# Kernel optimization log

Measured on AMD Instinct MI355X. Metric: run time of the kernel, lower is better.

Reference implementation:

```python
import jax, jax.numpy as jnp
import numpy as np

B, T = 32, 512
IN, D, H, HD, L, FFN = 375, 512, 8, 64, 6, 1024
NC, CD, LAT, K = 4, 64, 256, 512
DL, DH, DFF, OUT = 4, 512, 1024, 291


def setup_inputs() -> dict:
    key = jax.random.key(0)
    ks = iter(jax.random.split(key, 64))
    def p(shape, scale=0.02):
        return jax.random.normal(next(ks), shape, jnp.float32) * scale
    return {
        "x": jax.random.normal(next(ks), (B, T, IN), jnp.float32),
        "in_w": p((IN, D)), "in_b": jnp.zeros((D,), jnp.float32),
        "enc_ln1_s": jnp.ones((L, D), jnp.float32), "enc_ln1_b": jnp.zeros((L, D), jnp.float32),
        "enc_qkv_w": p((L, D, 3 * D)), "enc_qkv_b": jnp.zeros((L, 3 * D), jnp.float32),
        "enc_out_w": p((L, D, D)), "enc_out_b": jnp.zeros((L, D), jnp.float32),
        "enc_ln2_s": jnp.ones((L, D), jnp.float32), "enc_ln2_b": jnp.zeros((L, D), jnp.float32),
        "enc_ff1_w": p((L, D, FFN)), "enc_ff1_b": jnp.zeros((L, FFN), jnp.float32),
        "enc_ff2_w": p((L, FFN, D)), "enc_ff2_b": jnp.zeros((L, D), jnp.float32),
        "lat_w": p((D, LAT)), "lat_b": jnp.zeros((LAT,), jnp.float32),
        "codebook": jax.random.uniform(next(ks), (K, CD), jnp.float32, -1.0 / K, 1.0 / K),
        "unlat_w": p((LAT, DH)), "unlat_b": jnp.zeros((DH,), jnp.float32),
        "dec_ln_s": jnp.ones((DL, DH), jnp.float32), "dec_ln_b": jnp.zeros((DL, DH), jnp.float32),
        "dec_ff1_w": p((DL, DH, DFF)), "dec_ff1_b": jnp.zeros((DL, DFF), jnp.float32),
        "dec_ff2_w": p((DL, DFF, DH)), "dec_ff2_b": jnp.zeros((DL, DH), jnp.float32),
        "out_w": p((DH, OUT)), "out_b": jnp.zeros((OUT,), jnp.float32),
    }


def _ln(x, s, b):
    m = x.mean(-1, keepdims=True)
    v = jnp.var(x, axis=-1, keepdims=True)
    return (x - m) / jnp.sqrt(v + 1e-5) * s + b


def _rope(x, cos, sin):
    # interleaved even/odd rotation, matches torch stack(...,-1).flatten(-2)
    xe, xo = x[..., 0::2], x[..., 1::2]
    re = xe * cos - xo * sin
    ro = xe * sin + xo * cos
    return jnp.stack((re, ro), axis=-1).reshape(x.shape)


def _forward(x, in_w, in_b, enc_ln1_s, enc_ln1_b, enc_qkv_w, enc_qkv_b,
             enc_out_w, enc_out_b, enc_ln2_s, enc_ln2_b, enc_ff1_w, enc_ff1_b,
             enc_ff2_w, enc_ff2_b, lat_w, lat_b, codebook, unlat_w, unlat_b,
             dec_ln_s, dec_ln_b, dec_ff1_w, dec_ff1_b, dec_ff2_w, dec_ff2_b,
             out_w, out_b):
    h = x @ in_w + in_b  # [B,T,D]
    inv_freq = 1.0 / (10000.0 ** (jnp.arange(0, HD, 2, dtype=jnp.float32) / HD))
    freqs = jnp.outer(jnp.arange(T, dtype=jnp.float32), inv_freq)  # [T, HD/2]
    cos, sin = jnp.cos(freqs), jnp.sin(freqs)
    for i in range(L):
        y = _ln(h, enc_ln1_s[i], enc_ln1_b[i])
        qkv = (y @ enc_qkv_w[i] + enc_qkv_b[i]).reshape(B, T, 3, H, HD)
        qkv = qkv.transpose(2, 0, 3, 1, 4)  # [3,B,H,T,HD]
        q, k, v = qkv[0], qkv[1], qkv[2]
        q = _rope(q, cos, sin)
        k = _rope(k, cos, sin)
        sc = jnp.einsum('bhqd,bhkd->bhqk', q, k) / np.float32(np.sqrt(HD))
        probs = jax.nn.softmax(sc, axis=-1)
        a = jnp.einsum('bhqk,bhkd->bhqd', probs, v)
        a = a.transpose(0, 2, 1, 3).reshape(B, T, D)
        h = h + (a @ enc_out_w[i] + enc_out_b[i])
        y = _ln(h, enc_ln2_s[i], enc_ln2_b[i])
        h = h + (jax.nn.gelu(y @ enc_ff1_w[i] + enc_ff1_b[i], approximate=False)
                 @ enc_ff2_w[i] + enc_ff2_b[i])
    # VQ bottleneck: split each token latent into NC subvectors, nearest code each
    z_bt = (h @ lat_w + lat_b).reshape(B * T, LAT)
    flat_z = z_bt.reshape(-1, CD)  # [B*T*NC, CD]
    d = ((flat_z ** 2).sum(1, keepdims=True)
         - 2.0 * (flat_z @ codebook.T)
         + (codebook ** 2).sum(1))  # [B*T*NC, K]
    idx = jnp.argmin(d, axis=1)
    q_bt = codebook[idx].reshape(B * T, LAT)
    st = z_bt + jax.lax.stop_gradient(q_bt - z_bt)  # straight-through
    g = st.reshape(B, T, LAT) @ unlat_w + unlat_b
    for i in range(DL):
        y = _ln(g, dec_ln_s[i], dec_ln_b[i])
        g = g + (jax.nn.gelu(y @ dec_ff1_w[i] + dec_ff1_b[i], approximate=False)
                 @ dec_ff2_w[i] + dec_ff2_b[i])
    return g @ out_w + out_b  # [B,T,291]


def reference(x, in_w, in_b, enc_ln1_s, enc_ln1_b, enc_qkv_w, enc_qkv_b,
              enc_out_w, enc_out_b, enc_ln2_s, enc_ln2_b, enc_ff1_w, enc_ff1_b,
              enc_ff2_w, enc_ff2_b, lat_w, lat_b, codebook, unlat_w, unlat_b,
              dec_ln_s, dec_ln_b, dec_ff1_w, dec_ff1_b, dec_ff2_w, dec_ff2_b,
              out_w, out_b):
    return _forward(x, in_w, in_b, enc_ln1_s, enc_ln1_b, enc_qkv_w, enc_qkv_b,
                    enc_out_w, enc_out_b, enc_ln2_s, enc_ln2_b, enc_ff1_w, enc_ff1_b,
                    enc_ff2_w, enc_ff2_b, lat_w, lat_b, codebook, unlat_w, unlat_b,
                    dec_ln_s, dec_ln_b, dec_ff1_w, dec_ff1_b, dec_ff2_w, dec_ff2_b,
                    out_w, out_b)
```

## Files before the change

kernel.cpp:

```cpp
#include <hip/hip_runtime.h>
#include <hip/hip_bf16.h>

#define BB 32
#define TT 512
#define IND 375
#define DD 512
#define HH 8
#define HDD 64
#define LL 6
#define FFNN 1024
#define LATD 256
#define KCODES 512
#define DLL 4
#define DHH 512
#define DFFF 1024
#define OUTD 291
#define MTOK (BB*TT)
#define KPAD 384
#define NPAD 384

__global__ void rope_table_k(float* __restrict__ cosb, float* __restrict__ sinb) {
  int idx = blockIdx.x * blockDim.x + threadIdx.x;
  if (idx >= TT * 32) return;
  int t = idx >> 5, i = idx & 31;
  float inv = powf(10000.0f, -(float)(2 * i) / 64.0f);
  float f = (float)t * inv;
  cosb[idx] = cosf(f);
  sinb[idx] = sinf(f);
}

__global__ void pad_x_k(const float* __restrict__ x, float* __restrict__ Xp) {
  int m = blockIdx.x;
  const float* src = x + (size_t)m * IND;
  float* dst = Xp + (size_t)m * KPAD;
  for (int k = threadIdx.x; k < KPAD; k += 256)
    dst[k] = (k < IND) ? src[k] : 0.0f;
}
__global__ void pad_wx_k(const float* __restrict__ w, float* __restrict__ Wp) {
  int e = blockIdx.x * 256 + threadIdx.x;
  if (e >= KPAD * DD) return;
  int k = e >> 9, n = e & 511;
  Wp[e] = (k < IND) ? w[(size_t)k * DD + n] : 0.0f;
}
__global__ void pad_wo_k(const float* __restrict__ w, const float* __restrict__ b,
                         float* __restrict__ Wp, float* __restrict__ bp) {
  int e = blockIdx.x * 256 + threadIdx.x;
  if (e >= DHH * NPAD) return;
  int k = e / NPAD, n = e - k * NPAD;
  Wp[e] = (n < OUTD) ? w[(size_t)k * OUTD + n] : 0.0f;
  if (e < NPAD) bp[e] = (e < OUTD) ? b[e] : 0.0f;
}
__global__ void unpad_k(const float* __restrict__ Cp, float* __restrict__ out) {
  int m = blockIdx.x;
  const float* src = Cp + (size_t)m * NPAD;
  float* dst = out + (size_t)m * OUTD;
  for (int n = threadIdx.x; n < OUTD; n += 256)
    dst[n] = src[n];
}

template<int EPI>
__global__ __launch_bounds__(256) void gemm128_k(const float* __restrict__ A,
                                                 const float* __restrict__ W,
                                                 const float* __restrict__ bias,
                                                 const float* __restrict__ R,
                                                 float* __restrict__ C,
                                                 int M, int K, int N,
                                                 const float* __restrict__ COS,
                                                 const float* __restrict__ SIN) {
  __shared__ float As[32][128];
  __shared__ float4 Bs4[32][2][16];
  const int bn = blockIdx.x * 128;
  const int bm = blockIdx.y * 128;
  const int tid = threadIdx.x;
  const int tx = tid & 15;
  const int ty = tid >> 4;
  const int ar = tid >> 1;
  const int ak = (tid & 1) * 16;
  const int bk = tid >> 3;
  const int bxs = tid & 7;

  float acc[8][8] = {};

  for (int k0 = 0; k0 < K; k0 += 32) {
    const float* ap = A + (size_t)(bm + ar) * K + k0 + ak;
    float4 a0 = *(const float4*)ap;
    float4 a1 = *(const float4*)(ap + 4);
    float4 a2 = *(const float4*)(ap + 8);
    float4 a3 = *(const float4*)(ap + 12);
    const float* bp = W + (size_t)(k0 + bk) * N + bn + bxs * 16;
    float4 b0 = *(const float4*)bp;
    float4 b1 = *(const float4*)(bp + 4);
    float4 b2 = *(const float4*)(bp + 8);
    float4 b3 = *(const float4*)(bp + 12);

    __syncthreads();
    As[ak +  0][ar] = a0.x; As[ak +  1][ar] = a0.y; As[ak +  2][ar] = a0.z; As[ak +  3][ar] = a0.w;
    As[ak +  4][ar] = a1.x; As[ak +  5][ar] = a1.y; As[ak +  6][ar] = a1.z; As[ak +  7][ar] = a1.w;
    As[ak +  8][ar] = a2.x; As[ak +  9][ar] = a2.y; As[ak + 10][ar] = a2.z; As[ak + 11][ar] = a2.w;
    As[ak + 12][ar] = a3.x; As[ak + 13][ar] = a3.y; As[ak + 14][ar] = a3.z; As[ak + 15][ar] = a3.w;
    Bs4[bk][0][2 * bxs]     = b0;
    Bs4[bk][1][2 * bxs]     = b1;
    Bs4[bk][0][2 * bxs + 1] = b2;
    Bs4[bk][1][2 * bxs + 1] = b3;
    __syncthreads();

#pragma unroll
    for (int kk = 0; kk < 32; ++kk) {
      float4 va0 = *(const float4*)&As[kk][ty * 8];
      float4 va1 = *(const float4*)&As[kk][ty * 8 + 4];
      float4 vb0 = Bs4[kk][0][tx];
      float4 vb1 = Bs4[kk][1][tx];
      float av[8] = {va0.x, va0.y, va0.z, va0.w, va1.x, va1.y, va1.z, va1.w};
      float bv[8] = {vb0.x, vb0.y, vb0.z, vb0.w, vb1.x, vb1.y, vb1.z, vb1.w};
#pragma unroll
      for (int ii = 0; ii < 8; ++ii)
#pragma unroll
        for (int jj = 0; jj < 8; ++jj)
          acc[ii][jj] = __builtin_fmaf(av[ii], bv[jj], acc[ii][jj]);
    }
  }

#pragma unroll
  for (int ii = 0; ii < 8; ++ii) {
    int m = bm + ty * 8 + ii;
#pragma unroll
    for (int g = 0; g < 2; ++g) {
      int n0 = bn + tx * 8 + g * 4;
      float t4[4];
#pragma unroll
      for (int j = 0; j < 4; ++j) {
        float v = acc[ii][g * 4 + j] + bias[n0 + j];
        if (EPI == 1) v += R[(size_t)m * N + n0 + j];
        if (EPI == 2) v = 0.5f * v * (1.0f + erff(v * 0.70710678118654752f));
        t4[j] = v;
      }
      if (EPI == 3 && n0 < 2 * DD) {
        int tpos = m & 511;
        int i0 = (n0 & 63) >> 1;
        float c0 = COS[tpos * 32 + i0],     s0 = SIN[tpos * 32 + i0];
        float c1 = COS[tpos * 32 + i0 + 1], s1 = SIN[tpos * 32 + i0 + 1];
        float xe0 = t4[0], xo0 = t4[1], xe1 = t4[2], xo1 = t4[3];
        t4[0] = xe0 * c0 - xo0 * s0;
        t4[1] = xe0 * s0 + xo0 * c0;
        t4[2] = xe1 * c1 - xo1 * s1;
        t4[3] = xe1 * s1 + xo1 * c1;
      }
      float4 vv; vv.x = t4[0]; vv.y = t4[1]; vv.z = t4[2]; vv.w = t4[3];
      *(float4*)&C[(size_t)m * N + n0] = vv;
    }
  }
}

__global__ __launch_bounds__(256) void ln_k(const float* __restrict__ X,
                                            const float* __restrict__ s,
                                            const float* __restrict__ b,
                                            float* __restrict__ Y) {
  int wave = threadIdx.x >> 6, lane = threadIdx.x & 63;
  int row = blockIdx.x * 4 + wave;
  const float* x = X + (size_t)row * DD;
  float v[8];
  float sum = 0.0f;
#pragma unroll
  for (int j = 0; j < 8; ++j) { v[j] = x[lane + 64 * j]; sum += v[j]; }
#pragma unroll
  for (int o = 32; o; o >>= 1) sum += __shfl_xor(sum, o);
  float mean = sum * (1.0f / 512.0f);
  float var = 0.0f;
#pragma unroll
  for (int j = 0; j < 8; ++j) { float d = v[j] - mean; var += d * d; }
#pragma unroll
  for (int o = 32; o; o >>= 1) var += __shfl_xor(var, o);
  float inv = 1.0f / sqrtf(var * (1.0f / 512.0f) + 1e-5f);
  float* y = Y + (size_t)row * DD;
#pragma unroll
  for (int j = 0; j < 8; ++j) {
    int d = lane + 64 * j;
    y[d] = (v[j] - mean) * inv * s[d] + b[d];
  }
}

__global__ __launch_bounds__(256) void fattn_k(const float* __restrict__ qkv,
                                               float* __restrict__ out) {
  __shared__ float Qs[64][68];
  __shared__ float KVs[64][68];
  __shared__ float Ps[64][68];
  const int tid = threadIdx.x;
  const int tx = tid & 15, ty = tid >> 4;
  const int g = blockIdx.x;
  const int xcd = g & 7, slot = g >> 3;
  const int qt = slot & 7;
  const int p = ((slot >> 3) << 3) | xcd;
  const int h = p & 7;
  const int b = p >> 3;
  const float* base = qkv + (size_t)b * TT * (3 * DD) + h * HDD;

  {
    int r = tid & 63, q0 = tid >> 6;
#pragma unroll
    for (int jj = 0; jj < 4; ++jj) {
      int q = q0 + jj * 4;
      float4 v = *(const float4*)(base + (size_t)(qt * 64 + r) * (3 * DD) + q * 4);
      Qs[q * 4 + 0][r] = v.x; Qs[q * 4 + 1][r] = v.y;
      Qs[q * 4 + 2][r] = v.z; Qs[q * 4 + 3][r] = v.w;
    }
  }

  float o[4][4] = {};
  float m[4] = {-1e30f, -1e30f, -1e30f, -1e30f};
  float l[4] = {0.f, 0.f, 0.f, 0.f};

  for (int kt = 0; kt < 8; ++kt) {
    __syncthreads();
    {
      int r = tid & 63, q0 = tid >> 6;
#pragma unroll
      for (int jj = 0; jj < 4; ++jj) {
        int q = q0 + jj * 4;
        float4 v = *(const float4*)(base + (size_t)(kt * 64 + r) * (3 * DD) + DD + q * 4);
        KVs[q * 4 + 0][r] = v.x; KVs[q * 4 + 1][r] = v.y;
        KVs[q * 4 + 2][r] = v.z; KVs[q * 4 + 3][r] = v.w;
      }
    }
    __syncthreads();

    float s[4][4] = {};
#pragma unroll 4
    for (int d = 0; d < 64; ++d) {
      float4 a4 = *(const float4*)&Qs[d][ty * 4];
      float4 b4 = *(const float4*)&KVs[d][tx * 4];
      float av[4] = {a4.x, a4.y, a4.z, a4.w};
      float bv[4] = {b4.x, b4.y, b4.z, b4.w};
#pragma unroll
      for (int ii = 0; ii < 4; ++ii)
#pragma unroll
        for (int jj = 0; jj < 4; ++jj)
          s[ii][jj] = __builtin_fmaf(av[ii], bv[jj], s[ii][jj]);
    }

#pragma unroll
    for (int i = 0; i < 4; ++i) {
      float mm = fmaxf(fmaxf(s[i][0], s[i][1]), fmaxf(s[i][2], s[i][3])) * 0.125f;
#pragma unroll
      for (int off = 1; off < 16; off <<= 1) mm = fmaxf(mm, __shfl_xor(mm, off));
      float mn = fmaxf(m[i], mm);
      float f = expf(m[i] - mn);
      m[i] = mn;
      float ls = 0.0f;
#pragma unroll
      for (int j = 0; j < 4; ++j) {
        float pp = expf(__builtin_fmaf(s[i][j], 0.125f, -mn));
        s[i][j] = pp;
        ls += pp;
      }
#pragma unroll
      for (int off = 1; off < 16; off <<= 1) ls += __shfl_xor(ls, off);
      l[i] = __builtin_fmaf(l[i], f, ls);
#pragma unroll
      for (int j = 0; j < 4; ++j) o[i][j] *= f;
    }

    __syncthreads();

#pragma unroll
    for (int j = 0; j < 4; ++j) {
      float4 pv; pv.x = s[0][j]; pv.y = s[1][j]; pv.z = s[2][j]; pv.w = s[3][j];
      *(float4*)&Ps[tx * 4 + j][ty * 4] = pv;
    }
#pragma unroll
    for (int ii = 0; ii < 4; ++ii) {
      int e = tid + 256 * ii;
      int c = e >> 4, q = e & 15;
      float4 v = *(const float4*)(base + (size_t)(kt * 64 + c) * (3 * DD) + 2 * DD + q * 4);
      *(float4*)&KVs[c][q * 4] = v;
    }
    __syncthreads();

#pragma unroll 4
    for (int c = 0; c < 64; ++c) {
      float4 a4 = *(const float4*)&Ps[c][ty * 4];
      float4 b4 = *(const float4*)&KVs[c][tx * 4];
      float av[4] = {a4.x, a4.y, a4.z, a4.w};
      float bv[4] = {b4.x, b4.y, b4.z, b4.w};
#pragma unroll
      for (int ii = 0; ii < 4; ++ii)
#pragma unroll
        for (int jj = 0; jj < 4; ++jj)
          o[ii][jj] = __builtin_fmaf(av[ii], bv[jj], o[ii][jj]);
    }
  }

#pragma unroll
  for (int i = 0; i < 4; ++i) {
    float inv = 1.0f / l[i];
    int tok = b * TT + qt * 64 + ty * 4 + i;
    float4 vv;
    vv.x = o[i][0] * inv; vv.y = o[i][1] * inv;
    vv.z = o[i][2] * inv; vv.w = o[i][3] * inv;
    *(float4*)&out[(size_t)tok * DD + h * HDD + tx * 4] = vv;
  }
}

__device__ __forceinline__ float npsumsq64(const float* __restrict__ a) {
  float r0 = __fmul_rn(a[0], a[0]), r1 = __fmul_rn(a[1], a[1]);
  float r2 = __fmul_rn(a[2], a[2]), r3 = __fmul_rn(a[3], a[3]);
  float r4 = __fmul_rn(a[4], a[4]), r5 = __fmul_rn(a[5], a[5]);
  float r6 = __fmul_rn(a[6], a[6]), r7 = __fmul_rn(a[7], a[7]);
#pragma unroll
  for (int i = 8; i < 64; i += 8) {
    r0 = __fadd_rn(r0, __fmul_rn(a[i + 0], a[i + 0]));
    r1 = __fadd_rn(r1, __fmul_rn(a[i + 1], a[i + 1]));
    r2 = __fadd_rn(r2, __fmul_rn(a[i + 2], a[i + 2]));
    r3 = __fadd_rn(r3, __fmul_rn(a[i + 3], a[i + 3]));
    r4 = __fadd_rn(r4, __fmul_rn(a[i + 4], a[i + 4]));
    r5 = __fadd_rn(r5, __fmul_rn(a[i + 5], a[i + 5]));
    r6 = __fadd_rn(r6, __fmul_rn(a[i + 6], a[i + 6]));
    r7 = __fadd_rn(r7, __fmul_rn(a[i + 7], a[i + 7]));
  }
  return __fadd_rn(__fadd_rn(__fadd_rn(r0, r1), __fadd_rn(r2, r3)),
                   __fadd_rn(__fadd_rn(r4, r5), __fadd_rn(r6, r7)));
}

__global__ void vqs2_k(const float* __restrict__ CB, float* __restrict__ S2) {
  int k = blockIdx.x * 256 + threadIdx.x;
  if (k < KCODES) S2[k] = npsumsq64(CB + (size_t)k * 64);
}

__global__ __launch_bounds__(256) void vq32b_k(const float* __restrict__ Z,
                                               const float* __restrict__ CB,
                                               const float* __restrict__ S2,
                                               int* __restrict__ idxOut) {
  __shared__ float zs[16][68];
  __shared__ float cs[64][68];
  __shared__ float s2s[64];
  __shared__ float rv[256];
  __shared__ int   ri[256];
  const int tid = threadIdx.x;
  const int lr = tid >> 4;
  const int sub = tid & 15;
  const int row0 = blockIdx.x * 16;

  {
    int r = tid >> 4, q = tid & 15;
    *(float4*)&zs[r][q * 4] = *(const float4*)(Z + (size_t)(row0 + r) * 64 + q * 4);
  }
  __syncthreads();

  const float S1 = npsumsq64(zs[lr]);

  float bv = 3.4e38f;
  int bi = 0x7fffffff;
  for (int ct = 0; ct < 8; ++ct) {
    __syncthreads();
    for (int e = tid; e < 1024; e += 256) {
      int r = e >> 4, q = e & 15;
      *(float4*)&cs[r][q * 4] = *(const float4*)(CB + (size_t)(ct * 64 + r) * 64 + q * 4);
    }
    if (tid < 64) s2s[tid] = S2[ct * 64 + tid];
    __syncthreads();
#pragma unroll
    for (int cc = 0; cc < 4; ++cc) {
      int kl = cc * 16 + sub;
      float g = 0.0f;
#pragma unroll
      for (int d4 = 0; d4 < 16; ++d4) {
        float4 zf = *(const float4*)&zs[lr][d4 * 4];
        float4 cf = *(const float4*)&cs[kl][d4 * 4];
        g = __builtin_fmaf(zf.x, cf.x, g);
        g = __builtin_fmaf(zf.y, cf.y, g);
        g = __builtin_fmaf(zf.z, cf.z, g);
        g = __builtin_fmaf(zf.w, cf.w, g);
      }
      float d32 = __fadd_rn(__fsub_rn(S1, __fmul_rn(2.0f, g)), s2s[kl]);
      int k = ct * 64 + kl;
      if (d32 < bv || (d32 == bv && k < bi)) { bv = d32; bi = k; }
    }
  }
  rv[tid] = bv; ri[tid] = bi;
  __syncthreads();
  if (sub == 0) {
    float bb = rv[tid]; int ii = ri[tid];
#pragma unroll
    for (int j = 1; j < 16; ++j) {
      float v = rv[tid + j]; int id = ri[tid + j];
      if (v < bb || (v == bb && id < ii)) { bb = v; ii = id; }
    }
    idxOut[row0 + lr] = ii;
  }
}

__global__ void stgather_k(const float* __restrict__ Z, const float* __restrict__ CB,
                           const int* __restrict__ idx, float* __restrict__ Q) {
  int e = blockIdx.x * blockDim.x + threadIdx.x;
  if (e >= MTOK * LATD) return;
  int chunk = e >> 6, d = e & 63;
  int k = idx[chunk] & (KCODES - 1);
  float z = Z[e];
  float c = CB[(size_t)k * 64 + d];
  Q[e] = __fadd_rn(z, __fsub_rn(c, z));
}

static inline dim3 g128(int M, int N) { return dim3(N / 128, M / 128); }

extern "C" void kernel_launch(void* const* d_in, const int* in_sizes, int n_in,
                              void* d_out, int out_size, void* d_ws, size_t ws_size,
                              hipStream_t stream) {
  const float* x        = (const float*)d_in[0];
  const float* in_w     = (const float*)d_in[1];
  const float* in_b     = (const float*)d_in[2];
  const float* ln1_s    = (const float*)d_in[3];
  const float* ln1_b    = (const float*)d_in[4];
  const float* qkv_w    = (const float*)d_in[5];
  const float* qkv_b    = (const float*)d_in[6];
  const float* aout_w   = (const float*)d_in[7];
  const float* aout_b   = (const float*)d_in[8];
  const float* ln2_s    = (const float*)d_in[9];
  const float* ln2_b    = (const float*)d_in[10];
  const float* ff1_w    = (const float*)d_in[11];
  const float* ff1_b    = (const float*)d_in[12];
  const float* ff2_w    = (const float*)d_in[13];
  const float* ff2_b    = (const float*)d_in[14];
  const float* lat_w    = (const float*)d_in[15];
  const float* lat_b    = (const float*)d_in[16];
  const float* codebook = (const float*)d_in[17];
  const float* unlat_w  = (const float*)d_in[18];
  const float* unlat_b  = (const float*)d_in[19];
  const float* dln_s    = (const float*)d_in[20];
  const float* dln_b    = (const float*)d_in[21];
  const float* dff1_w   = (const float*)d_in[22];
  const float* dff1_b   = (const float*)d_in[23];
  const float* dff2_w   = (const float*)d_in[24];
  const float* dff2_b   = (const float*)d_in[25];
  const float* ow       = (const float*)d_in[26];
  const float* ob       = (const float*)d_in[27];
  float* out = (float*)d_out;

  float* ws   = (float*)d_ws;
  float* Hb   = ws;
  float* Yb   = Hb + (size_t)MTOK * DD;
  float* QKVb = Yb + (size_t)MTOK * DD;
  float* COSb = QKVb + (size_t)MTOK * 3 * DD;
  float* SINb = COSb + TT * 32;
  int*   IDXb = (int*)(SINb + TT * 32);
  float* S2b  = (float*)(IDXb + MTOK * 4);
  float* WXp  = S2b + KCODES;
  float* WOp  = WXp + (size_t)KPAD * DD;
  float* BOp  = WOp + (size_t)DHH * NPAD;
  float* Xp   = QKVb;
  float* Cp   = QKVb;

  dim3 blk(256);

  rope_table_k<<<(TT * 32 + 255) / 256, blk, 0, stream>>>(COSb, SINb);
  vqs2_k<<<2, blk, 0, stream>>>(codebook, S2b);
  pad_wx_k<<<(KPAD * DD + 255) / 256, blk, 0, stream>>>(in_w, WXp);
  pad_wo_k<<<(DHH * NPAD + 255) / 256, blk, 0, stream>>>(ow, ob, WOp, BOp);
  pad_x_k<<<MTOK, blk, 0, stream>>>(x, Xp);

  gemm128_k<0><<<g128(MTOK, DD), blk, 0, stream>>>(Xp, WXp, in_b, nullptr, Hb,
                                                   MTOK, KPAD, DD, nullptr, nullptr);

  for (int l = 0; l < LL; ++l) {
    ln_k<<<MTOK / 4, blk, 0, stream>>>(Hb, ln1_s + l * DD, ln1_b + l * DD, Yb);
    gemm128_k<3><<<g128(MTOK, 3 * DD), blk, 0, stream>>>(Yb, qkv_w + (size_t)l * DD * 3 * DD,
                                                         qkv_b + l * 3 * DD, nullptr, QKVb,
                                                         MTOK, DD, 3 * DD, COSb, SINb);
    fattn_k<<<BB * HH * (TT / 64), blk, 0, stream>>>(QKVb, Yb);
    gemm128_k<1><<<g128(MTOK, DD), blk, 0, stream>>>(Yb, aout_w + (size_t)l * DD * DD,
                                                     aout_b + l * DD, Hb, Hb, MTOK, DD, DD,
                                                     nullptr, nullptr);
    ln_k<<<MTOK / 4, blk, 0, stream>>>(Hb, ln2_s + l * DD, ln2_b + l * DD, Yb);
    gemm128_k<2><<<g128(MTOK, FFNN), blk, 0, stream>>>(Yb, ff1_w + (size_t)l * DD * FFNN,
                                                       ff1_b + l * FFNN, nullptr, QKVb,
                                                       MTOK, DD, FFNN, nullptr, nullptr);
    gemm128_k<1><<<g128(MTOK, DD), blk, 0, stream>>>(QKVb, ff2_w + (size_t)l * FFNN * DD,
                                                     ff2_b + l * DD, Hb, Hb, MTOK, FFNN, DD,
                                                     nullptr, nullptr);
  }

  gemm128_k<0><<<g128(MTOK, LATD), blk, 0, stream>>>(Hb, lat_w, lat_b, nullptr, Yb,
                                                     MTOK, DD, LATD, nullptr, nullptr);
  vq32b_k<<<(MTOK * 4) / 16, blk, 0, stream>>>(Yb, codebook, S2b, IDXb);
  stgather_k<<<(MTOK * LATD) / 256, blk, 0, stream>>>(Yb, codebook, IDXb, QKVb);
  gemm128_k<0><<<g128(MTOK, DHH), blk, 0, stream>>>(QKVb, unlat_w, unlat_b, nullptr, Hb,
                                                    MTOK, LATD, DHH, nullptr, nullptr);

  for (int l = 0; l < DLL; ++l) {
    ln_k<<<MTOK / 4, blk, 0, stream>>>(Hb, dln_s + l * DHH, dln_b + l * DHH, Yb);
    gemm128_k<2><<<g128(MTOK, DFFF), blk, 0, stream>>>(Yb, dff1_w + (size_t)l * DHH * DFFF,
                                                       dff1_b + l * DFFF, nullptr, QKVb,
                                                       MTOK, DHH, DFFF, nullptr, nullptr);
    gemm128_k<1><<<g128(MTOK, DHH), blk, 0, stream>>>(QKVb, dff2_w + (size_t)l * DFFF * DHH,
                                                      dff2_b + l * DHH, Hb, Hb, MTOK, DFFF, DHH,
                                                      nullptr, nullptr);
  }

  gemm128_k<0><<<g128(MTOK, NPAD), blk, 0, stream>>>(Hb, WOp, BOp, nullptr, Cp,
                                                     MTOK, DHH, NPAD, nullptr, nullptr);
  unpad_k<<<MTOK, blk, 0, stream>>>(Cp, out);
}
```

Before: 8.868 ms.

## Use split-bf16 MFMA GEMM for decoder and output projections

Adds a bf16x3 (hi/lo split) MFMA GEMM kernel and routes the unlatent, decoder FFN and output projections through it, with weights pre-split and transposed into bf16 hi/lo buffers. A tiles are split on the fly while being staged into LDS. The aim is to replace the scalar fp32 FMA GEMM with matrix-core throughput while keeping near-fp32 accuracy. The cost is extra split kernels per call, three MFMAs per product, and more workspace; the encoder GEMMs stay on the old path.

```diff
diff --git a/kernel.cpp b/kernel.cpp
--- a/kernel.cpp
+++ b/kernel.cpp
@@ -19,6 +19,18 @@
 #define KPAD 384
 #define NPAD 384
 
+typedef short short8v __attribute__((ext_vector_type(8)));
+typedef float float4v __attribute__((ext_vector_type(4)));
+
+__device__ __forceinline__ unsigned short f2bf(float f) {
+  unsigned int u = __float_as_uint(f);
+  unsigned int r = (u + 0x7FFFu + ((u >> 16) & 1u)) >> 16;
+  return (unsigned short)r;
+}
+__device__ __forceinline__ float bf2f(unsigned short s) {
+  return __uint_as_float(((unsigned int)s) << 16);
+}
+
 __global__ void rope_table_k(float* __restrict__ cosb, float* __restrict__ sinb) {
   int idx = blockIdx.x * blockDim.x + threadIdx.x;
   if (idx >= TT * 32) return;
@@ -56,6 +68,18 @@
   float* dst = out + (size_t)m * OUTD;
   for (int n = threadIdx.x; n < OUTD; n += 256)
     dst[n] = src[n];
+}
+
+__global__ void wsplit_k(const float* __restrict__ w, unsigned short* __restrict__ hiT,
+                         unsigned short* __restrict__ loT, int K, int N) {
+  int e = blockIdx.x * 256 + threadIdx.x;
+  if (e >= K * N) return;
+  int k = e / N, n = e - k * N;
+  float a = w[e];
+  unsigned short h = f2bf(a);
+  unsigned short l = f2bf(a - bf2f(h));
+  hiT[(size_t)n * K + k] = h;
+  loT[(size_t)n * K + k] = l;
 }
 
 template<int EPI>
@@ -147,6 +171,101 @@
       }
       float4 vv; vv.x = t4[0]; vv.y = t4[1]; vv.z = t4[2]; vv.w = t4[3];
       *(float4*)&C[(size_t)m * N + n0] = vv;
+    }
+  }
+}
+
+template<int EPI>
+__global__ __launch_bounds__(256) void bgemm_k(const float* __restrict__ A,
+                                               const unsigned short* __restrict__ BhiT,
+                                               const unsigned short* __restrict__ BloT,
+                                               const float* __restrict__ bias,
+                                               const float* __restrict__ R,
+                                               float* __restrict__ C,
+                                               int M, int K, int N) {
+  __shared__ unsigned short Ah[128][40];
+  __shared__ unsigned short Al[128][40];
+  __shared__ unsigned short Bh[128][40];
+  __shared__ unsigned short Bl[128][40];
+  const int bn = blockIdx.x * 128;
+  const int bm = blockIdx.y * 128;
+  const int tid = threadIdx.x;
+  const int w = tid >> 6, lane = tid & 63;
+  const int wm = (w >> 1) * 64, wn = (w & 1) * 64;
+  const int lr = lane & 15;
+  const int kh = lane >> 4;
+
+  const int sr = tid >> 1;
+  const int sk = (tid & 1) * 16;
+
+  float4v acc[4][4] = {};
+
+  for (int k0 = 0; k0 < K; k0 += 32) {
+    const float* ap = A + (size_t)(bm + sr) * K + k0 + sk;
+    float av[16];
+#pragma unroll
+    for (int q = 0; q < 4; ++q) {
+      float4 v = *(const float4*)(ap + q * 4);
+      av[q * 4 + 0] = v.x; av[q * 4 + 1] = v.y; av[q * 4 + 2] = v.z; av[q * 4 + 3] = v.w;
+    }
+    const unsigned short* bph = BhiT + (size_t)(bn + sr) * K + k0 + sk;
+    const unsigned short* bpl = BloT + (size_t)(bn + sr) * K + k0 + sk;
+    uint4 bh0 = *(const uint4*)bph, bh1 = *(const uint4*)(bph + 8);
+    uint4 bl0 = *(const uint4*)bpl, bl1 = *(const uint4*)(bpl + 8);
+
+    __syncthreads();
+    unsigned int hw[8], lw[8];
+#pragma unroll
+    for (int q = 0; q < 8; ++q) {
+      unsigned short h0 = f2bf(av[2 * q]);
+      unsigned short l0 = f2bf(av[2 * q] - bf2f(h0));
+      unsigned short h1 = f2bf(av[2 * q + 1]);
+      unsigned short l1 = f2bf(av[2 * q + 1] - bf2f(h1));
+      hw[q] = (unsigned int)h0 | ((unsigned int)h1 << 16);
+      lw[q] = (unsigned int)l0 | ((unsigned int)l1 << 16);
+    }
+    *(uint4*)&Ah[sr][sk]     = make_uint4(hw[0], hw[1], hw[2], hw[3]);
+    *(uint4*)&Ah[sr][sk + 8] = make_uint4(hw[4], hw[5], hw[6], hw[7]);
+    *(uint4*)&Al[sr][sk]     = make_uint4(lw[0], lw[1], lw[2], lw[3]);
+    *(uint4*)&Al[sr][sk + 8] = make_uint4(lw[4], lw[5], lw[6], lw[7]);
+    *(uint4*)&Bh[sr][sk]     = bh0;
+    *(uint4*)&Bh[sr][sk + 8] = bh1;
+    *(uint4*)&Bl[sr][sk]     = bl0;
+    *(uint4*)&Bl[sr][sk + 8] = bl1;
+    __syncthreads();
+
+    short8v bfh[4], bfl[4];
+#pragma unroll
+    for (int nt = 0; nt < 4; ++nt) {
+      bfh[nt] = *(const short8v*)&Bh[wn + nt * 16 + lr][kh * 8];
+      bfl[nt] = *(const short8v*)&Bl[wn + nt * 16 + lr][kh * 8];
+    }
+#pragma unroll
+    for (int mt = 0; mt < 4; ++mt) {
+      short8v afh = *(const short8v*)&Ah[wm + mt * 16 + lr][kh * 8];
+      short8v afl = *(const short8v*)&Al[wm + mt * 16 + lr][kh * 8];
+#pragma unroll
+      for (int nt = 0; nt < 4; ++nt) {
+        acc[mt][nt] = __builtin_amdgcn_mfma_f32_16x16x32_bf16(afh, bfh[nt], acc[mt][nt], 0, 0, 0);
+        acc[mt][nt] = __builtin_amdgcn_mfma_f32_16x16x32_bf16(afh, bfl[nt], acc[mt][nt], 0, 0, 0);
+        acc[mt][nt] = __builtin_amdgcn_mfma_f32_16x16x32_bf16(afl, bfh[nt], acc[mt][nt], 0, 0, 0);
+      }
+    }
+  }
+
+#pragma unroll
+  for (int mt = 0; mt < 4; ++mt) {
+#pragma unroll
+    for (int nt = 0; nt < 4; ++nt) {
+#pragma unroll
+      for (int r = 0; r < 4; ++r) {
+        int row = bm + wm + mt * 16 + (lane >> 4) * 4 + r;
+        int col = bn + wn + nt * 16 + (lane & 15);
+        float v = acc[mt][nt][r] + bias[col];
+        if (EPI == 1) v += R[(size_t)row * N + col];
+        if (EPI == 2) v = 0.5f * v * (1.0f + erff(v * 0.70710678118654752f));
+        C[(size_t)row * N + col] = v;
+      }
     }
   }
 }
@@ -445,8 +564,17 @@
   float* WXp  = S2b + KCODES;
   float* WOp  = WXp + (size_t)KPAD * DD;
   float* BOp  = WOp + (size_t)DHH * NPAD;
-  float* Xp   = QKVb;
-  float* Cp   = QKVb;
+  unsigned short* u0  = (unsigned short*)(BOp + NPAD);
+  unsigned short* UH  = u0;
+  unsigned short* UL  = UH + (size_t)DHH * LATD;
+  unsigned short* F1H = UL + (size_t)DHH * LATD;
+  unsigned short* F1L = F1H + (size_t)DLL * DFFF * DHH;
+  unsigned short* F2H = F1L + (size_t)DLL * DFFF * DHH;
+  unsigned short* F2L = F2H + (size_t)DLL * DHH * DFFF;
+  unsigned short* OH  = F2L + (size_t)DLL * DHH * DFFF;
+  unsigned short* OL  = OH + (size_t)NPAD * DHH;
+  float* Xp = QKVb;
+  float* Cp = QKVb;
 
   dim3 blk(256);
 
@@ -455,6 +583,17 @@
   pad_wx_k<<<(KPAD * DD + 255) / 256, blk, 0, stream>>>(in_w, WXp);
   pad_wo_k<<<(DHH * NPAD + 255) / 256, blk, 0, stream>>>(ow, ob, WOp, BOp);
   pad_x_k<<<MTOK, blk, 0, stream>>>(x, Xp);
+
+  wsplit_k<<<(LATD * DHH + 255) / 256, blk, 0, stream>>>(unlat_w, UH, UL, LATD, DHH);
+  for (int l = 0; l < DLL; ++l) {
+    wsplit_k<<<(DHH * DFFF + 255) / 256, blk, 0, stream>>>(
+        dff1_w + (size_t)l * DHH * DFFF, F1H + (size_t)l * DFFF * DHH,
+        F1L + (size_t)l * DFFF * DHH, DHH, DFFF);
+    wsplit_k<<<(DFFF * DHH + 255) / 256, blk, 0, stream>>>(
+        dff2_w + (size_t)l * DFFF * DHH, F2H + (size_t)l * DHH * DFFF,
+        F2L + (size_t)l * DHH * DFFF, DFFF, DHH);
+  }
+  wsplit_k<<<(DHH * NPAD + 255) / 256, blk, 0, stream>>>(WOp, OH, OL, DHH, NPAD);
 
   gemm128_k<0><<<g128(MTOK, DD), blk, 0, stream>>>(Xp, WXp, in_b, nullptr, Hb,
                                                    MTOK, KPAD, DD, nullptr, nullptr);
@@ -481,20 +620,21 @@
                                                      MTOK, DD, LATD, nullptr, nullptr);
   vq32b_k<<<(MTOK * 4) / 16, blk, 0, stream>>>(Yb, codebook, S2b, IDXb);
   stgather_k<<<(MTOK * LATD) / 256, blk, 0, stream>>>(Yb, codebook, IDXb, QKVb);
-  gemm128_k<0><<<g128(MTOK, DHH), blk, 0, stream>>>(QKVb, unlat_w, unlat_b, nullptr, Hb,
-                                                    MTOK, LATD, DHH, nullptr, nullptr);
-
+
+  bgemm_k<0><<<g128(MTOK, DHH), blk, 0, stream>>>(QKVb, UH, UL, unlat_b, nullptr, Hb,
+                                                  MTOK, LATD, DHH);
   for (int l = 0; l < DLL; ++l) {
     ln_k<<<MTOK / 4, blk, 0, stream>>>(Hb, dln_s + l * DHH, dln_b + l * DHH, Yb);
-    gemm128_k<2><<<g128(MTOK, DFFF), blk, 0, stream>>>(Yb, dff1_w + (size_t)l * DHH * DFFF,
-                                                       dff1_b + l * DFFF, nullptr, QKVb,
-                                                       MTOK, DHH, DFFF, nullptr, nullptr);
-    gemm128_k<1><<<g128(MTOK, DHH), blk, 0, stream>>>(QKVb, dff2_w + (size_t)l * DFFF * DHH,
-                                                      dff2_b + l * DHH, Hb, Hb, MTOK, DFFF, DHH,
-                                                      nullptr, nullptr);
-  }
-
-  gemm128_k<0><<<g128(MTOK, NPAD), blk, 0, stream>>>(Hb, WOp, BOp, nullptr, Cp,
-                                                     MTOK, DHH, NPAD, nullptr, nullptr);
+    bgemm_k<2><<<g128(MTOK, DFFF), blk, 0, stream>>>(Yb, F1H + (size_t)l * DFFF * DHH,
+                                                     F1L + (size_t)l * DFFF * DHH,
+                                                     dff1_b + l * DFFF, nullptr, QKVb,
+                                                     MTOK, DHH, DFFF);
+    bgemm_k<1><<<g128(MTOK, DHH), blk, 0, stream>>>(QKVb, F2H + (size_t)l * DHH * DFFF,
+                                                    F2L + (size_t)l * DHH * DFFF,
+                                                    dff2_b + l * DHH, Hb, Hb,
+                                                    MTOK, DFFF, DHH);
+  }
+  bgemm_k<0><<<g128(MTOK, NPAD), blk, 0, stream>>>(Hb, OH, OL, BOp, nullptr, Cp,
+                                                   MTOK, DHH, NPAD);
   unpad_k<<<MTOK, blk, 0, stream>>>(Cp, out);
 }
```

After: 7.821 ms (median of 2 runs). 1.13x faster.

## Emulate fp32 GEMMs with three-way bf16 split on MFMA

Applied to the files above, without the earlier changes.

Adds a bf16x3 split-precision GEMM that decomposes activations on the fly and weights in a pre-pass into three bf16 planes, then accumulates six MFMA cross products in fp32. All dense layers use this path when the workspace is large enough, with the old fp32 SIMT GEMM kept as a fallback. The aim is to move GEMM work off vector ALUs onto matrix cores. The cost is extra weight conversion kernels each call, a large workspace, and a small accuracy difference from dropping the lowest-order terms.

```diff
diff --git a/kernel.cpp b/kernel.cpp
--- a/kernel.cpp
+++ b/kernel.cpp
@@ -19,6 +19,18 @@
 #define KPAD 384
 #define NPAD 384
 
+typedef short short8v __attribute__((ext_vector_type(8)));
+typedef float float4v __attribute__((ext_vector_type(4)));
+
+__device__ __forceinline__ unsigned short f2bf(float f) {
+  unsigned int u = __float_as_uint(f);
+  unsigned int r = (u + 0x7FFFu + ((u >> 16) & 1u)) >> 16;
+  return (unsigned short)r;
+}
+__device__ __forceinline__ float bf2f(unsigned short s) {
+  return __uint_as_float(((unsigned int)s) << 16);
+}
+
 __global__ void rope_table_k(float* __restrict__ cosb, float* __restrict__ sinb) {
   int idx = blockIdx.x * blockDim.x + threadIdx.x;
   if (idx >= TT * 32) return;
@@ -56,6 +68,23 @@
   float* dst = out + (size_t)m * OUTD;
   for (int n = threadIdx.x; n < OUTD; n += 256)
     dst[n] = src[n];
+}
+
+__global__ void wsplit3_k(const float* __restrict__ w, unsigned short* __restrict__ o,
+                          size_t planeSz, int K, int N) {
+  int e = blockIdx.x * 256 + threadIdx.x;
+  if (e >= K * N) return;
+  int k = e / N, n = e - k * N;
+  float a = w[e];
+  unsigned short h0 = f2bf(a);
+  float r = a - bf2f(h0);
+  unsigned short h1 = f2bf(r);
+  float r2 = r - bf2f(h1);
+  unsigned short h2 = f2bf(r2);
+  size_t off = (size_t)n * K + k;
+  o[off] = h0;
+  o[planeSz + off] = h1;
+  o[2 * planeSz + off] = h2;
 }
 
 template<int EPI>
@@ -147,6 +176,121 @@
       }
       float4 vv; vv.x = t4[0]; vv.y = t4[1]; vv.z = t4[2]; vv.w = t4[3];
       *(float4*)&C[(size_t)m * N + n0] = vv;
+    }
+  }
+}
+
+template<int EPI>
+__global__ __launch_bounds__(256) void bgemm6_k(const float* __restrict__ A,
+                                                const unsigned short* __restrict__ BT,
+                                                size_t planeSz,
+                                                const float* __restrict__ bias,
+                                                const float* __restrict__ R,
+                                                float* __restrict__ C,
+                                                int M, int K, int N,
+                                                const float* __restrict__ COS,
+                                                const float* __restrict__ SIN) {
+  __shared__ unsigned short A0s[128][40], A1s[128][40], A2s[128][40];
+  __shared__ unsigned short B0s[128][40], B1s[128][40], B2s[128][40];
+  const int bn = blockIdx.x * 128;
+  const int bm = blockIdx.y * 128;
+  const int tid = threadIdx.x;
+  const int w = tid >> 6, lane = tid & 63;
+  const int wm = (w >> 1) * 64, wn = (w & 1) * 64;
+  const int lr = lane & 15;
+  const int kh = lane >> 4;
+  const int sr = tid >> 1;
+  const int sk = (tid & 1) * 16;
+
+  float4v acc[4][4] = {};
+
+  for (int k0 = 0; k0 < K; k0 += 32) {
+    const float* ap = A + (size_t)(bm + sr) * K + k0 + sk;
+    float av[16];
+#pragma unroll
+    for (int q = 0; q < 4; ++q) {
+      float4 v = *(const float4*)(ap + q * 4);
+      av[q * 4 + 0] = v.x; av[q * 4 + 1] = v.y; av[q * 4 + 2] = v.z; av[q * 4 + 3] = v.w;
+    }
+    const unsigned short* b0p = BT + (size_t)(bn + sr) * K + k0 + sk;
+    uint4 b00 = *(const uint4*)b0p, b01 = *(const uint4*)(b0p + 8);
+    const unsigned short* b1p = b0p + planeSz;
+    uint4 b10 = *(const uint4*)b1p, b11 = *(const uint4*)(b1p + 8);
+    const unsigned short* b2p = b1p + planeSz;
+    uint4 b20 = *(const uint4*)b2p, b21 = *(const uint4*)(b2p + 8);
+
+    __syncthreads();
+    unsigned int w0[8], w1[8], w2[8];
+#pragma unroll
+    for (int q = 0; q < 8; ++q) {
+      float aa = av[2 * q], ab = av[2 * q + 1];
+      unsigned short h0a = f2bf(aa); float ra = aa - bf2f(h0a);
+      unsigned short h1a = f2bf(ra); float r2a = ra - bf2f(h1a);
+      unsigned short h2a = f2bf(r2a);
+      unsigned short h0b = f2bf(ab); float rb = ab - bf2f(h0b);
+      unsigned short h1b = f2bf(rb); float r2b = rb - bf2f(h1b);
+      unsigned short h2b = f2bf(r2b);
+      w0[q] = (unsigned int)h0a | ((unsigned int)h0b << 16);
+      w1[q] = (unsigned int)h1a | ((unsigned int)h1b << 16);
+      w2[q] = (unsigned int)h2a | ((unsigned int)h2b << 16);
+    }
+    *(uint4*)&A0s[sr][sk]     = make_uint4(w0[0], w0[1], w0[2], w0[3]);
+    *(uint4*)&A0s[sr][sk + 8] = make_uint4(w0[4], w0[5], w0[6], w0[7]);
+    *(uint4*)&A1s[sr][sk]     = make_uint4(w1[0], w1[1], w1[2], w1[3]);
+    *(uint4*)&A1s[sr][sk + 8] = make_uint4(w1[4], w1[5], w1[6], w1[7]);
+    *(uint4*)&A2s[sr][sk]     = make_uint4(w2[0], w2[1], w2[2], w2[3]);
+    *(uint4*)&A2s[sr][sk + 8] = make_uint4(w2[4], w2[5], w2[6], w2[7]);
+    *(uint4*)&B0s[sr][sk]     = b00;  *(uint4*)&B0s[sr][sk + 8] = b01;
+    *(uint4*)&B1s[sr][sk]     = b10;  *(uint4*)&B1s[sr][sk + 8] = b11;
+    *(uint4*)&B2s[sr][sk]     = b20;  *(uint4*)&B2s[sr][sk + 8] = b21;
+    __syncthreads();
+
+    short8v b0f[4], b1f[4], b2f[4];
+#pragma unroll
+    for (int nt = 0; nt < 4; ++nt) {
+      b0f[nt] = *(const short8v*)&B0s[wn + nt * 16 + lr][kh * 8];
+      b1f[nt] = *(const short8v*)&B1s[wn + nt * 16 + lr][kh * 8];
+      b2f[nt] = *(const short8v*)&B2s[wn + nt * 16 + lr][kh * 8];
+    }
+#pragma unroll
+    for (int mt = 0; mt < 4; ++mt) {
+      short8v a0f = *(const short8v*)&A0s[wm + mt * 16 + lr][kh * 8];
+      short8v a1f = *(const short8v*)&A1s[wm + mt * 16 + lr][kh * 8];
+      short8v a2f = *(const short8v*)&A2s[wm + mt * 16 + lr][kh * 8];
+#pragma unroll
+      for (int nt = 0; nt < 4; ++nt) {
+        acc[mt][nt] = __builtin_amdgcn_mfma_f32_16x16x32_bf16(a0f, b0f[nt], acc[mt][nt], 0, 0, 0);
+        acc[mt][nt] = __builtin_amdgcn_mfma_f32_16x16x32_bf16(a0f, b1f[nt], acc[mt][nt], 0, 0, 0);
+        acc[mt][nt] = __builtin_amdgcn_mfma_f32_16x16x32_bf16(a1f, b0f[nt], acc[mt][nt], 0, 0, 0);
+        acc[mt][nt] = __builtin_amdgcn_mfma_f32_16x16x32_bf16(a0f, b2f[nt], acc[mt][nt], 0, 0, 0);
+        acc[mt][nt] = __builtin_amdgcn_mfma_f32_16x16x32_bf16(a1f, b1f[nt], acc[mt][nt], 0, 0, 0);
+        acc[mt][nt] = __builtin_amdgcn_mfma_f32_16x16x32_bf16(a2f, b0f[nt], acc[mt][nt], 0, 0, 0);
+      }
+    }
+  }
+
+#pragma unroll
+  for (int mt = 0; mt < 4; ++mt) {
+#pragma unroll
+    for (int nt = 0; nt < 4; ++nt) {
+      int col = bn + wn + nt * 16 + (lane & 15);
+#pragma unroll
+      for (int r = 0; r < 4; ++r) {
+        int row = bm + wm + mt * 16 + (lane >> 4) * 4 + r;
+        float v = acc[mt][nt][r] + bias[col];
+        if (EPI == 1) v += R[(size_t)row * N + col];
+        if (EPI == 2) v = 0.5f * v * (1.0f + erff(v * 0.70710678118654752f));
+        if (EPI == 3) {
+          float p = __shfl_xor(v, 1);
+          if (col < 2 * DD) {
+            int tpos = row & 511;
+            int i0 = (col & 63) >> 1;
+            float c = COS[tpos * 32 + i0], s = SIN[tpos * 32 + i0];
+            v = ((col & 1) == 0) ? (v * c - p * s) : (p * s + v * c);
+          }
+        }
+        C[(size_t)row * N + col] = v;
+      }
     }
   }
 }
@@ -448,6 +592,29 @@
   float* Xp   = QKVb;
   float* Cp   = QKVb;
 
+  uintptr_t ua = ((uintptr_t)(BOp + NPAD) + 15) & ~(uintptr_t)15;
+  unsigned short* Uw = (unsigned short*)ua;
+  const size_t QWp = (size_t)(3 * DD) * DD;
+  const size_t AWp = (size_t)DD * DD;
+  const size_t F1p = (size_t)DFFF * DHH;
+  const size_t F2p = (size_t)DHH * DFFF;
+  const size_t INp = (size_t)DD * KPAD;
+  const size_t LTp = (size_t)LATD * DD;
+  const size_t UWp = (size_t)DHH * LATD;
+  const size_t OWp = (size_t)NPAD * DHH;
+  unsigned short* QW  = Uw;
+  unsigned short* AW  = QW  + 6 * 3 * QWp;
+  unsigned short* F1  = AW  + 6 * 3 * AWp;
+  unsigned short* F2  = F1  + 6 * 3 * F1p;
+  unsigned short* INW = F2  + 6 * 3 * F2p;
+  unsigned short* LTW = INW + 3 * INp;
+  unsigned short* UW  = LTW + 3 * LTp;
+  unsigned short* D1  = UW  + 3 * UWp;
+  unsigned short* D2  = D1  + 4 * 3 * F1p;
+  unsigned short* OW  = D2  + 4 * 3 * F2p;
+  size_t need = (size_t)((char*)(OW + 3 * OWp) - (char*)d_ws) + 64;
+  const bool mf = ws_size >= need;
+
   dim3 blk(256);
 
   rope_table_k<<<(TT * 32 + 255) / 256, blk, 0, stream>>>(COSb, SINb);
@@ -456,45 +623,103 @@
   pad_wo_k<<<(DHH * NPAD + 255) / 256, blk, 0, stream>>>(ow, ob, WOp, BOp);
   pad_x_k<<<MTOK, blk, 0, stream>>>(x, Xp);
 
-  gemm128_k<0><<<g128(MTOK, DD), blk, 0, stream>>>(Xp, WXp, in_b, nullptr, Hb,
-                                                   MTOK, KPAD, DD, nullptr, nullptr);
-
-  for (int l = 0; l < LL; ++l) {
-    ln_k<<<MTOK / 4, blk, 0, stream>>>(Hb, ln1_s + l * DD, ln1_b + l * DD, Yb);
-    gemm128_k<3><<<g128(MTOK, 3 * DD), blk, 0, stream>>>(Yb, qkv_w + (size_t)l * DD * 3 * DD,
-                                                         qkv_b + l * 3 * DD, nullptr, QKVb,
-                                                         MTOK, DD, 3 * DD, COSb, SINb);
-    fattn_k<<<BB * HH * (TT / 64), blk, 0, stream>>>(QKVb, Yb);
-    gemm128_k<1><<<g128(MTOK, DD), blk, 0, stream>>>(Yb, aout_w + (size_t)l * DD * DD,
-                                                     aout_b + l * DD, Hb, Hb, MTOK, DD, DD,
-                                                     nullptr, nullptr);
-    ln_k<<<MTOK / 4, blk, 0, stream>>>(Hb, ln2_s + l * DD, ln2_b + l * DD, Yb);
-    gemm128_k<2><<<g128(MTOK, FFNN), blk, 0, stream>>>(Yb, ff1_w + (size_t)l * DD * FFNN,
-                                                       ff1_b + l * FFNN, nullptr, QKVb,
-                                                       MTOK, DD, FFNN, nullptr, nullptr);
-    gemm128_k<1><<<g128(MTOK, DD), blk, 0, stream>>>(QKVb, ff2_w + (size_t)l * FFNN * DD,
-                                                     ff2_b + l * DD, Hb, Hb, MTOK, FFNN, DD,
-                                                     nullptr, nullptr);
-  }
-
-  gemm128_k<0><<<g128(MTOK, LATD), blk, 0, stream>>>(Hb, lat_w, lat_b, nullptr, Yb,
-                                                     MTOK, DD, LATD, nullptr, nullptr);
-  vq32b_k<<<(MTOK * 4) / 16, blk, 0, stream>>>(Yb, codebook, S2b, IDXb);
-  stgather_k<<<(MTOK * LATD) / 256, blk, 0, stream>>>(Yb, codebook, IDXb, QKVb);
-  gemm128_k<0><<<g128(MTOK, DHH), blk, 0, stream>>>(QKVb, unlat_w, unlat_b, nullptr, Hb,
-                                                    MTOK, LATD, DHH, nullptr, nullptr);
-
-  for (int l = 0; l < DLL; ++l) {
-    ln_k<<<MTOK / 4, blk, 0, stream>>>(Hb, dln_s + l * DHH, dln_b + l * DHH, Yb);
-    gemm128_k<2><<<g128(MTOK, DFFF), blk, 0, stream>>>(Yb, dff1_w + (size_t)l * DHH * DFFF,
-                                                       dff1_b + l * DFFF, nullptr, QKVb,
-                                                       MTOK, DHH, DFFF, nullptr, nullptr);
-    gemm128_k<1><<<g128(MTOK, DHH), blk, 0, stream>>>(QKVb, dff2_w + (size_t)l * DFFF * DHH,
-                                                      dff2_b + l * DHH, Hb, Hb, MTOK, DFFF, DHH,
+  if (mf) {
+    for (int l = 0; l < LL; ++l) {
+      wsplit3_k<<<(int)((DD * 3 * DD + 255) / 256), blk, 0, stream>>>(
+          qkv_w + (size_t)l * DD * 3 * DD, QW + (size_t)l * 3 * QWp, QWp, DD, 3 * DD);
+      wsplit3_k<<<(int)((DD * DD + 255) / 256), blk, 0, stream>>>(
+          aout_w + (size_t)l * DD * DD, AW + (size_t)l * 3 * AWp, AWp, DD, DD);
+      wsplit3_k<<<(int)((DD * FFNN + 255) / 256), blk, 0, stream>>>(
+          ff1_w + (size_t)l * DD * FFNN, F1 + (size_t)l * 3 * F1p, F1p, DD, FFNN);
+      wsplit3_k<<<(int)((FFNN * DD + 255) / 256), blk, 0, stream>>>(
+          ff2_w + (size_t)l * FFNN * DD, F2 + (size_t)l * 3 * F2p, F2p, FFNN, DD);
+    }
+    wsplit3_k<<<(int)((KPAD * DD + 255) / 256), blk, 0, stream>>>(WXp, INW, INp, KPAD, DD);
+    wsplit3_k<<<(int)((DD * LATD + 255) / 256), blk, 0, stream>>>(lat_w, LTW, LTp, DD, LATD);
+    wsplit3_k<<<(int)((LATD * DHH + 255) / 256), blk, 0, stream>>>(unlat_w, UW, UWp, LATD, DHH);
+    for (int l = 0; l < DLL; ++l) {
+      wsplit3_k<<<(int)((DHH * DFFF + 255) / 256), blk, 0, stream>>>(
+          dff1_w + (size_t)l * DHH * DFFF, D1 + (size_t)l * 3 * F1p, F1p, DHH, DFFF);
+      wsplit3_k<<<(int)((DFFF * DHH + 255) / 256), blk, 0, stream>>>(
+          dff2_w + (size_t)l * DFFF * DHH, D2 + (size_t)l * 3 * F2p, F2p, DFFF, DHH);
+    }
+    wsplit3_k<<<(int)((DHH * NPAD + 255) / 256), blk, 0, stream>>>(WOp, OW, OWp, DHH, NPAD);
+
+    bgemm6_k<0><<<g128(MTOK, DD), blk, 0, stream>>>(Xp, INW, INp, in_b, nullptr, Hb,
+                                                    MTOK, KPAD, DD, nullptr, nullptr);
+    for (int l = 0; l < LL; ++l) {
+      ln_k<<<MTOK / 4, blk, 0, stream>>>(Hb, ln1_s + l * DD, ln1_b + l * DD, Yb);
+      bgemm6_k<3><<<g128(MTOK, 3 * DD), blk, 0, stream>>>(Yb, QW + (size_t)l * 3 * QWp, QWp,
+                                                          qkv_b + l * 3 * DD, nullptr, QKVb,
+                                                          MTOK, DD, 3 * DD, COSb, SINb);
+      fattn_k<<<BB * HH * (TT / 64), blk, 0, stream>>>(QKVb, Yb);
+      bgemm6_k<1><<<g128(MTOK, DD), blk, 0, stream>>>(Yb, AW + (size_t)l * 3 * AWp, AWp,
+                                                      aout_b + l * DD, Hb, Hb, MTOK, DD, DD,
                                                       nullptr, nullptr);
-  }
-
-  gemm128_k<0><<<g128(MTOK, NPAD), blk, 0, stream>>>(Hb, WOp, BOp, nullptr, Cp,
-                                                     MTOK, DHH, NPAD, nullptr, nullptr);
-  unpad_k<<<MTOK, blk, 0, stream>>>(Cp, out);
-}
+      ln_k<<<MTOK / 4, blk, 0, stream>>>(Hb, ln2_s + l * DD, ln2_b + l * DD, Yb);
+      bgemm6_k<2><<<g128(MTOK, FFNN), blk, 0, stream>>>(Yb, F1 + (size_t)l * 3 * F1p, F1p,
+                                                        ff1_b + l * FFNN, nullptr, QKVb,
+                                                        MTOK, DD, FFNN, nullptr, nullptr);
+      bgemm6_k<1><<<g128(MTOK, DD), blk, 0, stream>>>(QKVb, F2 + (size_t)l * 3 * F2p, F2p,
+                                                      ff2_b + l * DD, Hb, Hb, MTOK, FFNN, DD,
+                                                      nullptr, nullptr);
+    }
+    bgemm6_k<0><<<g128(MTOK, LATD), blk, 0, stream>>>(Hb, LTW, LTp, lat_b, nullptr, Yb,
+                                                      MTOK, DD, LATD, nullptr, nullptr);
+    vq32b_k<<<(MTOK * 4) / 16, blk, 0, stream>>>(Yb, codebook, S2b, IDXb);
+    stgather_k<<<(MTOK * LATD) / 256, blk, 0, stream>>>(Yb, codebook, IDXb, QKVb);
+
+    bgemm6_k<0><<<g128(MTOK, DHH), blk, 0, stream>>>(QKVb, UW, UWp, unlat_b, nullptr, Hb,
+                                                     MTOK, LATD, DHH, nullptr, nullptr);
+    for (int l = 0; l < DLL; ++l) {
+      ln_k<<<MTOK / 4, blk, 0, stream>>>(Hb, dln_s + l * DHH, dln_b + l * DHH, Yb);
+      bgemm6_k<2><<<g128(MTOK, DFFF), blk, 0, stream>>>(Yb, D1 + (size_t)l * 3 * F1p, F1p,
+                                                        dff1_b + l * DFFF, nullptr, QKVb,
+                                                        MTOK, DHH, DFFF, nullptr, nullptr);
+      bgemm6_k<1><<<g128(MTOK, DHH), blk, 0, stream>>>(QKVb, D2 + (size_t)l * 3 * F2p, F2p,
+                                                       dff2_b + l * DHH, Hb, Hb,
+                                                       MTOK, DFFF, DHH, nullptr, nullptr);
+    }
+    bgemm6_k<0><<<g128(MTOK, NPAD), blk, 0, stream>>>(Hb, OW, OWp, BOp, nullptr, Cp,
+                                                      MTOK, DHH, NPAD, nullptr, nullptr);
+    unpad_k<<<MTOK, blk, 0, stream>>>(Cp, out);
+  } else {
+    gemm128_k<0><<<g128(MTOK, DD), blk, 0, stream>>>(Xp, WXp, in_b, nullptr, Hb,
+                                                     MTOK, KPAD, DD, nullptr, nullptr);
+    for (int l = 0; l < LL; ++l) {
+      ln_k<<<MTOK / 4, blk, 0, stream>>>(Hb, ln1_s + l * DD, ln1_b + l * DD, Yb);
+      gemm128_k<3><<<g128(MTOK, 3 * DD), blk, 0, stream>>>(Yb, qkv_w + (size_t)l * DD * 3 * DD,
+                                                           qkv_b + l * 3 * DD, nullptr, QKVb,
+                                                           MTOK, DD, 3 * DD, COSb, SINb);
+      fattn_k<<<BB * HH * (TT / 64), blk, 0, stream>>>(QKVb, Yb);
+      gemm128_k<1><<<g128(MTOK, DD), blk, 0, stream>>>(Yb, aout_w + (size_t)l * DD * DD,
+                                                       aout_b + l * DD, Hb, Hb, MTOK, DD, DD,
+                                                       nullptr, nullptr);
+      ln_k<<<MTOK / 4, blk, 0, stream>>>(Hb, ln2_s + l * DD, ln2_b + l * DD, Yb);
+      gemm128_k<2><<<g128(MTOK, FFNN), blk, 0, stream>>>(Yb, ff1_w + (size_t)l * DD * FFNN,
+                                                         ff1_b + l * FFNN, nullptr, QKVb,
+                                                         MTOK, DD, FFNN, nullptr, nullptr);
+      gemm128_k<1><<<g128(MTOK, DD), blk, 0, stream>>>(QKVb, ff2_w + (size_t)l * FFNN * DD,
+                                                       ff2_b + l * DD, Hb, Hb, MTOK, FFNN, DD,
+                                                       nullptr, nullptr);
+    }
+    gemm128_k<0><<<g128(MTOK, LATD), blk, 0, stream>>>(Hb, lat_w, lat_b, nullptr, Yb,
+                                                       MTOK, DD, LATD, nullptr, nullptr);
+    vq32b_k<<<(MTOK * 4) / 16, blk, 0, stream>>>(Yb, codebook, S2b, IDXb);
+    stgather_k<<<(MTOK * LATD) / 256, blk, 0, stream>>>(Yb, codebook, IDXb, QKVb);
+    gemm128_k<0><<<g128(MTOK, DHH), blk, 0, stream>>>(QKVb, unlat_w, unlat_b, nullptr, Hb,
+                                                      MTOK, LATD, DHH, nullptr, nullptr);
+    for (int l = 0; l < DLL; ++l) {
+      ln_k<<<MTOK / 4, blk, 0, stream>>>(Hb, dln_s + l * DHH, dln_b + l * DHH, Yb);
+      gemm128_k<2><<<g128(MTOK, DFFF), blk, 0, stream>>>(Yb, dff1_w + (size_t)l * DHH * DFFF,
+                                                         dff1_b + l * DFFF, nullptr, QKVb,
+                                                         MTOK, DHH, DFFF, nullptr, nullptr);
+      gemm128_k<1><<<g128(MTOK, DHH), blk, 0, stream>>>(QKVb, dff2_w + (size_t)l * DFFF * DHH,
+                                                        dff2_b + l * DHH, Hb, Hb,
+                                                        MTOK, DFFF, DHH, nullptr, nullptr);
+    }
+    gemm128_k<0><<<g128(MTOK, NPAD), blk, 0, stream>>>(Hb, WOp, BOp, nullptr, Cp,
+                                                       MTOK, DHH, NPAD, nullptr, nullptr);
+    unpad_k<<<MTOK, blk, 0, stream>>>(Cp, out);
+  }
+}
```

Result: no change. 8.857 ms (-0.1%).
